# Performance work log

Measured on AMD Instinct MI355X. Metric: run time of the kernel, lower is better.

The kernel has to match this reference:

```python
import jax, jax.numpy as jnp
import numpy as np

N_NODES = 50000
N_EDGES = 800000
IN_CH = 128
HID = 32
HEADS = 8
OUT_CH = 40
NEG_SLOPE = 0.2


def setup_inputs() -> dict:
    key = jax.random.key(0)
    ks = jax.random.split(key, 12)
    g = lambda k, shape, fan: (jax.random.normal(k, shape, jnp.float32) / np.sqrt(fan).astype(np.float32))
    return {
        "x": jax.random.normal(ks[0], (N_NODES, IN_CH), jnp.float32),
        "edge_index": jax.random.randint(ks[1], (2, N_EDGES), 0, N_NODES, jnp.int64),
        "W1l": g(ks[2], (IN_CH, HEADS * HID), IN_CH),
        "W1r": g(ks[3], (IN_CH, HEADS * HID), IN_CH),
        "att1": g(ks[4], (HEADS, HID), HID),
        "b1": jnp.zeros((HEADS * HID,), jnp.float32),
        "W2l": g(ks[5], (HEADS * HID, HID), HEADS * HID),
        "W2r": g(ks[6], (HEADS * HID, HID), HEADS * HID),
        "att2": g(ks[7], (1, HID), HID),
        "b2": jnp.zeros((HID,), jnp.float32),
        "Wc": g(ks[8], (HID + IN_CH, OUT_CH), HID + IN_CH),
        "bc": jnp.zeros((OUT_CH,), jnp.float32),
    }


def _gatv2(x, ei, Wl, Wr, att, b, heads, ch):
    # GATv2Conv (concat=True): e_ij = att . LeakyReLU(Wl x_j + Wr x_i)
    n = x.shape[0]
    src, dst = ei[0], ei[1]  # message flows src(j) -> dst(i)
    xl = (x @ Wl).reshape(n, heads, ch)  # source transform
    xr = (x @ Wr).reshape(n, heads, ch)  # target transform
    e = jax.nn.leaky_relu(xl[src] + xr[dst], NEG_SLOPE)  # [E, H, C]
    score = jnp.einsum("ehc,hc->eh", e, att)             # [E, H]
    # per-target-node segment softmax (stable)
    m = jax.ops.segment_max(score, dst, num_segments=n)
    alpha = jnp.exp(score - m[dst])
    denom = jax.ops.segment_sum(alpha, dst, num_segments=n)
    alpha = alpha / denom[dst]
    out = jax.ops.segment_sum(alpha[:, :, None] * xl[src], dst, num_segments=n)
    return out.reshape(n, heads * ch) + b


def reference(x, edge_index, W1l, W1r, att1, b1, W2l, W2r, att2, b2, Wc, bc):
    n = x.shape[0]
    ar = jnp.arange(n, dtype=edge_index.dtype)
    ei = jnp.concatenate([edge_index, jnp.stack([ar, ar])], axis=1)  # add self-loops
    h1 = jax.nn.elu(_gatv2(x, ei, W1l, W1r, att1, b1, HEADS, HID))
    h2 = jax.nn.elu(_gatv2(h1, ei, W2l, W2r, att2, b2, 1, HID))
    combined = jnp.concatenate([h2, x], axis=1)
    return combined @ Wc + bc
```

## Files before the change

### kernel.cpp

```cpp
#include <hip/hip_runtime.h>
#include <cstdint>
#include <cstddef>
#include <math.h>

#define NN 50000
#define INCH 128
#define HIDC 32
#define NHEAD 8
#define OUTC 40

typedef unsigned short ushort_t;
using bf16x8 = __attribute__((ext_vector_type(8))) short;
using f32x4  = __attribute__((ext_vector_type(4))) float;

__device__ __forceinline__ float bf2f(unsigned short h) {
    return __uint_as_float(((unsigned int)h) << 16);
}
__device__ __forceinline__ unsigned short f2bf(float f) {
    unsigned int u = __float_as_uint(f);
    u = u + 0x7FFFu + ((u >> 16) & 1u);
    return (unsigned short)(u >> 16);
}
__device__ __forceinline__ float lo16(unsigned int u) { return __uint_as_float(u << 16); }
__device__ __forceinline__ float hi16(unsigned int u) { return __uint_as_float(u & 0xffff0000u); }

__global__ __launch_bounds__(256) void prep_all(
    const float* __restrict__ x, ushort_t* __restrict__ xb, int total8,
    const float* __restrict__ W1l, const float* __restrict__ W1r,
    const float* __restrict__ W2l, const float* __restrict__ W2r,
    const float* __restrict__ Wc,
    ushort_t* __restrict__ BT1, ushort_t* __restrict__ BT2, ushort_t* __restrict__ BTc,
    const int* __restrict__ ei, int E, int n, int* __restrict__ deg, int CX) {
    const int blk = blockIdx.x;
    const int tid = threadIdx.x;
    if (blk < CX) {
        int i = blk * 256 + tid;
        if (i >= total8) return;
        float4 f0 = *(const float4*)(x + (size_t)i * 8);
        float4 f1 = *(const float4*)(x + (size_t)i * 8 + 4);
        ushort4 u0, u1;
        u0.x = f2bf(f0.x); u0.y = f2bf(f0.y); u0.z = f2bf(f0.z); u0.w = f2bf(f0.w);
        u1.x = f2bf(f1.x); u1.y = f2bf(f1.y); u1.z = f2bf(f1.z); u1.w = f2bf(f1.w);
        *(ushort4*)(xb + (size_t)i * 8) = u0;
        *(ushort4*)(xb + (size_t)i * 8 + 4) = u1;
    } else if (blk < CX + 616) {
        int b = blk - CX, k = tid;
        if (b < 512) {
            if (k < 128) {
                float v = (b < 256) ? W1l[(size_t)k * 256 + b] : W1r[(size_t)k * 256 + (b - 256)];
                BT1[(size_t)b * 128 + k] = f2bf(v);
            }
        } else if (b < 576) {
            int c = b - 512;
            float v = (c < 32) ? W2l[(size_t)k * 32 + c] : W2r[(size_t)k * 32 + (c - 32)];
            BT2[(size_t)c * 256 + k] = f2bf(v);
        } else {
            int c = b - 576;
            if (k < 160) BTc[(size_t)c * 160 + k] = f2bf(Wc[(size_t)k * 40 + c]);
        }
    } else {
        int e = (blk - CX - 616) * 256 + tid;
        if (e >= E + n) return;
        int dst = (e < E) ? ei[E + e] : (e - E);
        atomicAdd(&deg[dst], 1);
    }
}


__global__ __launch_bounds__(1024) void partial_scan(
    const int* __restrict__ deg, int* __restrict__ row_start,
    int* __restrict__ block_total, int n) {
    __shared__ int wsum[16];
    const int tid = threadIdx.x, lane = tid & 63, wid = tid >> 6;
    int i = blockIdx.x * 1024 + tid;
    int v = (i < n) ? deg[i] : 0;
    int s = v;
    #pragma unroll
    for (int off = 1; off < 64; off <<= 1) {
        int t = __shfl_up(s, off, 64);
        if (lane >= off) s += t;
    }
    if (lane == 63) wsum[wid] = s;
    __syncthreads();
    if (wid == 0) {
        int ws = (lane < 16) ? wsum[lane] : 0;
        #pragma unroll
        for (int off = 1; off < 16; off <<= 1) {
            int t = __shfl_up(ws, off, 64);
            if (lane >= off) ws += t;
        }
        if (lane < 16) wsum[lane] = ws;
    }
    __syncthreads();
    int wexcl = wid ? wsum[wid - 1] : 0;
    if (i < n) row_start[i] = wexcl + s - v;
    if (tid == 0) block_total[blockIdx.x] = wsum[15];
}

__global__ void totals_scan(const int* __restrict__ block_total, int* __restrict__ block_off,
                            int* __restrict__ row_start_n, int nb) {
    int j = threadIdx.x;
    int v = (j < nb) ? block_total[j] : 0;
    int s = v;
    #pragma unroll
    for (int off = 1; off < 64; off <<= 1) {
        int t = __shfl_up(s, off, 64);
        if (j >= off) s += t;
    }
    if (j < nb) block_off[j] = s - v;
    if (j == nb - 1) *row_start_n = s;
}

__global__ __launch_bounds__(1024) void add_off(int* __restrict__ row_start, int* __restrict__ cursor,
                                                const int* __restrict__ block_off, int n) {
    int i = blockIdx.x * 1024 + threadIdx.x;
    if (i >= n) return;
    int val = row_start[i] + block_off[blockIdx.x];
    row_start[i] = val;
    cursor[i] = val;
}

__global__ void scatter_edges(const int* __restrict__ ei, int E, int n,
                              int* __restrict__ cursor, int* __restrict__ csr_src) {
    int e = blockIdx.x * blockDim.x + threadIdx.x;
    if (e >= E + n) return;
    int src, dst;
    if (e < E) { src = ei[e]; dst = ei[E + e]; } else { src = dst = e - E; }
    int pos = atomicAdd(&cursor[dst], 1);
    csr_src[pos] = src;
}

__global__ __launch_bounds__(256) void gemm1_mfma(
    const ushort_t* __restrict__ xb, const ushort_t* __restrict__ BT1,
    ushort_t* __restrict__ xlr1, int M) {
    __shared__ ushort_t As[128][72];
    __shared__ ushort_t Bs[128][72];
    const int tid = threadIdx.x;
    const int rowBase = blockIdx.y * 128;
    const int c0 = blockIdx.x * 128;
    const int wid = tid >> 6, lane = tid & 63;
    const int wr = wid >> 1, wc = wid & 1;
    const int l15 = lane & 15, l4 = lane >> 4;
    f32x4 acc[4][4];
    #pragma unroll
    for (int i = 0; i < 4; ++i)
        #pragma unroll
        for (int j = 0; j < 4; ++j)
            #pragma unroll
            for (int q = 0; q < 4; ++q) acc[i][j][q] = 0.f;

    for (int c = 0; c < 2; ++c) {
        #pragma unroll
        for (int h = 0; h < 4; ++h) {
            int idx = h * 256 + tid;
            int r = idx >> 3, seg = idx & 7;
            int row = rowBase + r;
            uint4 v = {0, 0, 0, 0};
            if (row < M) v = *(const uint4*)(xb + (size_t)row * 128 + c * 64 + seg * 8);
            *(uint4*)&As[r][seg * 8] = v;
            *(uint4*)&Bs[r][seg * 8] = *(const uint4*)(BT1 + (size_t)(c0 + r) * 128 + c * 64 + seg * 8);
        }
        __syncthreads();
        #pragma unroll
        for (int kk = 0; kk < 2; ++kk) {
            bf16x8 a[4], b[4];
            #pragma unroll
            for (int f = 0; f < 4; ++f) {
                a[f] = *(const bf16x8*)&As[wr * 64 + f * 16 + l15][kk * 32 + l4 * 8];
                b[f] = *(const bf16x8*)&Bs[wc * 64 + f * 16 + l15][kk * 32 + l4 * 8];
            }
            #pragma unroll
            for (int i = 0; i < 4; ++i)
                #pragma unroll
                for (int j = 0; j < 4; ++j)
                    acc[i][j] = __builtin_amdgcn_mfma_f32_16x16x32_bf16(a[i], b[j], acc[i][j], 0, 0, 0);
        }
        __syncthreads();
    }
    #pragma unroll
    for (int i = 0; i < 4; ++i)
        #pragma unroll
        for (int r = 0; r < 4; ++r) {
            int row = rowBase + wr * 64 + i * 16 + l4 * 4 + r;
            if (row >= M) continue;
            #pragma unroll
            for (int j = 0; j < 4; ++j) {
                int col = c0 + wc * 64 + j * 16 + l15;
                xlr1[(size_t)row * 512 + col] = f2bf(acc[i][j][r]);
            }
        }
}

__global__ __launch_bounds__(256) void dots1(
    const ushort_t* __restrict__ xlr, const float* __restrict__ att,
    float* __restrict__ dl, float* __restrict__ dr) {
    const int lane = threadIdx.x & 63;
    const int i = blockIdx.x * 4 + (threadIdx.x >> 6);
    const int l31 = lane & 31;
    const float4 atA = *(const float4*)(att + l31 * 8);
    const float4 atB = *(const float4*)(att + l31 * 8 + 4);
    ushort4 ua = *(const ushort4*)(xlr + (size_t)i * 512 + lane * 8);
    ushort4 ub = *(const ushort4*)(xlr + (size_t)i * 512 + lane * 8 + 4);
    float q = atA.x * bf2f(ua.x);
    q = fmaf(atA.y, bf2f(ua.y), q);
    q = fmaf(atA.z, bf2f(ua.z), q);
    q = fmaf(atA.w, bf2f(ua.w), q);
    q = fmaf(atB.x, bf2f(ub.x), q);
    q = fmaf(atB.y, bf2f(ub.y), q);
    q = fmaf(atB.z, bf2f(ub.z), q);
    q = fmaf(atB.w, bf2f(ub.w), q);
    q += __shfl_xor(q, 1);
    q += __shfl_xor(q, 2);
    if ((lane & 3) == 0) {
        int head = l31 >> 2;
        if (lane < 32) dl[(size_t)i * 8 + head] = q;
        else           dr[(size_t)i * 8 + head] = q;
    }
}

__global__ __launch_bounds__(256) void gat_agg1(
    const ushort_t* __restrict__ xlr, const float* __restrict__ dl,
    const float* __restrict__ dr, const float* __restrict__ att,
    const float* __restrict__ b,
    const int* __restrict__ row_start, const int* __restrict__ csr_src,
    ushort_t* __restrict__ h1) {
    const int lane = threadIdx.x & 63;
    const int i = blockIdx.x * 4 + (threadIdx.x >> 6);
    const int half = lane >> 5;
    const int sl = lane & 31;
    const int head = sl >> 2;

    uint4 xv = *(const uint4*)(xlr + (size_t)i * 512 + 256 + sl * 8);
    const float xr0 = lo16(xv.x), xr1 = hi16(xv.x), xr2 = lo16(xv.y), xr3 = hi16(xv.y);
    const float xr4 = lo16(xv.z), xr5 = hi16(xv.z), xr6 = lo16(xv.w), xr7 = hi16(xv.w);
    const float4 atA = *(const float4*)(att + sl * 8);
    const float4 atB = *(const float4*)(att + sl * 8 + 4);
    const float cbase = 0.6f * dr[(size_t)i * 8 + head];
    const int p0 = row_start[i], p1 = row_start[i + 1];

    float d = 0.f;
    float a0 = 0.f, a1 = 0.f, a2 = 0.f, a3 = 0.f, a4 = 0.f, a5 = 0.f, a6 = 0.f, a7 = 0.f;

    int pc = p0 + half; if (pc > p1 - 1) pc = p1 - 1;
    int j = csr_src[pc];
    uint4 uv = *(const uint4*)(xlr + (size_t)j * 512 + sl * 8);
    float dlj = dl[(size_t)j * 8 + head];

    for (int p = p0; p < p1; p += 2) {
        const bool val = (p + half) < p1;
        float v0 = lo16(uv.x), v1 = hi16(uv.x), v2 = lo16(uv.y), v3 = hi16(uv.y);
        float v4 = lo16(uv.z), v5 = hi16(uv.z), v6 = lo16(uv.w), v7 = hi16(uv.w);
        float base = fmaf(0.6f, dlj, cbase);
        int nxt = p + half + 2;
        if (nxt < p1) {
            int jn = csr_src[nxt];
            uv = *(const uint4*)(xlr + (size_t)jn * 512 + sl * 8);
            dlj = dl[(size_t)jn * 8 + head];
        }
        float q = atA.x * fabsf(v0 + xr0);
        q = fmaf(atA.y, fabsf(v1 + xr1), q);
        q = fmaf(atA.z, fabsf(v2 + xr2), q);
        q = fmaf(atA.w, fabsf(v3 + xr3), q);
        q = fmaf(atB.x, fabsf(v4 + xr4), q);
        q = fmaf(atB.y, fabsf(v5 + xr5), q);
        q = fmaf(atB.z, fabsf(v6 + xr6), q);
        q = fmaf(atB.w, fabsf(v7 + xr7), q);
        q += __shfl_xor(q, 1);
        q += __shfl_xor(q, 2);
        float w = val ? __expf(fmaf(0.4f, q, base)) : 0.f;
        d += w;
        a0 = fmaf(w, v0, a0); a1 = fmaf(w, v1, a1);
        a2 = fmaf(w, v2, a2); a3 = fmaf(w, v3, a3);
        a4 = fmaf(w, v4, a4); a5 = fmaf(w, v5, a5);
        a6 = fmaf(w, v6, a6); a7 = fmaf(w, v7, a7);
    }
    d  += __shfl_xor(d, 32);
    a0 += __shfl_xor(a0, 32); a1 += __shfl_xor(a1, 32);
    a2 += __shfl_xor(a2, 32); a3 += __shfl_xor(a3, 32);
    a4 += __shfl_xor(a4, 32); a5 += __shfl_xor(a5, 32);
    a6 += __shfl_xor(a6, 32); a7 += __shfl_xor(a7, 32);

    if (half == 0) {
        const float4 bA = *(const float4*)(b + sl * 8);
        const float4 bB = *(const float4*)(b + sl * 8 + 4);
        float inv = 1.f / d;
        float o0 = fmaf(a0, inv, bA.x), o1 = fmaf(a1, inv, bA.y);
        float o2 = fmaf(a2, inv, bA.z), o3 = fmaf(a3, inv, bA.w);
        float o4 = fmaf(a4, inv, bB.x), o5 = fmaf(a5, inv, bB.y);
        float o6 = fmaf(a6, inv, bB.z), o7 = fmaf(a7, inv, bB.w);
        o0 = o0 > 0.f ? o0 : __expf(o0) - 1.f;
        o1 = o1 > 0.f ? o1 : __expf(o1) - 1.f;
        o2 = o2 > 0.f ? o2 : __expf(o2) - 1.f;
        o3 = o3 > 0.f ? o3 : __expf(o3) - 1.f;
        o4 = o4 > 0.f ? o4 : __expf(o4) - 1.f;
        o5 = o5 > 0.f ? o5 : __expf(o5) - 1.f;
        o6 = o6 > 0.f ? o6 : __expf(o6) - 1.f;
        o7 = o7 > 0.f ? o7 : __expf(o7) - 1.f;
        uint4 ov;
        ov.x = ((unsigned)f2bf(o1) << 16) | f2bf(o0);
        ov.y = ((unsigned)f2bf(o3) << 16) | f2bf(o2);
        ov.z = ((unsigned)f2bf(o5) << 16) | f2bf(o4);
        ov.w = ((unsigned)f2bf(o7) << 16) | f2bf(o6);
        *(uint4*)(h1 + (size_t)i * 256 + sl * 8) = ov;
    }
}

__global__ __launch_bounds__(256) void gemm2_mfma(
    const ushort_t* __restrict__ h1, const ushort_t* __restrict__ BT2,
    ushort_t* __restrict__ xlr2, int M) {
    __shared__ ushort_t As[128][72];
    __shared__ ushort_t Bs[64][264];
    const int tid = threadIdx.x;
    const int rowBase = blockIdx.x * 128;
    const int wid = tid >> 6, lane = tid & 63;
    const int l15 = lane & 15, l4 = lane >> 4;
    #pragma unroll
    for (int h = 0; h < 8; ++h) {
        int idx = h * 256 + tid;
        int r = idx >> 5, seg = idx & 31;
        *(uint4*)&Bs[r][seg * 8] = *(const uint4*)(BT2 + (size_t)r * 256 + seg * 8);
    }
    f32x4 acc[2][4];
    #pragma unroll
    for (int i = 0; i < 2; ++i)
        #pragma unroll
        for (int j = 0; j < 4; ++j)
            #pragma unroll
            for (int q = 0; q < 4; ++q) acc[i][j][q] = 0.f;

    for (int c = 0; c < 4; ++c) {
        #pragma unroll
        for (int h = 0; h < 4; ++h) {
            int idx = h * 256 + tid;
            int r = idx >> 3, seg = idx & 7;
            int row = rowBase + r;
            uint4 v = {0, 0, 0, 0};
            if (row < M) v = *(const uint4*)(h1 + (size_t)row * 256 + c * 64 + seg * 8);
            *(uint4*)&As[r][seg * 8] = v;
        }
        __syncthreads();
        #pragma unroll
        for (int kk = 0; kk < 2; ++kk) {
            bf16x8 a[2], b[4];
            #pragma unroll
            for (int f = 0; f < 2; ++f)
                a[f] = *(const bf16x8*)&As[wid * 32 + f * 16 + l15][kk * 32 + l4 * 8];
            #pragma unroll
            for (int f = 0; f < 4; ++f)
                b[f] = *(const bf16x8*)&Bs[f * 16 + l15][c * 64 + kk * 32 + l4 * 8];
            #pragma unroll
            for (int i = 0; i < 2; ++i)
                #pragma unroll
                for (int j = 0; j < 4; ++j)
                    acc[i][j] = __builtin_amdgcn_mfma_f32_16x16x32_bf16(a[i], b[j], acc[i][j], 0, 0, 0);
        }
        __syncthreads();
    }
    #pragma unroll
    for (int i = 0; i < 2; ++i)
        #pragma unroll
        for (int r = 0; r < 4; ++r) {
            int row = rowBase + wid * 32 + i * 16 + l4 * 4 + r;
            if (row >= M) continue;
            #pragma unroll
            for (int j = 0; j < 4; ++j) {
                int col = j * 16 + l15;
                xlr2[(size_t)row * 64 + col] = f2bf(acc[i][j][r]);
            }
        }
}

__global__ __launch_bounds__(256) void dots2(
    const ushort_t* __restrict__ xlr, const float* __restrict__ att,
    float* __restrict__ dl, float* __restrict__ dr) {
    const int lane = threadIdx.x & 63;
    const int i = blockIdx.x * 8 + (threadIdx.x >> 6) * 2 + (lane >> 5);
    const int sub = lane & 31;
    const float2 at = *(const float2*)(att + (sub & 15) * 2);
    ushort2 u = *(const ushort2*)(xlr + (size_t)i * 64 + sub * 2);
    float q = at.x * bf2f(u.x);
    q = fmaf(at.y, bf2f(u.y), q);
    q += __shfl_xor(q, 1);
    q += __shfl_xor(q, 2);
    q += __shfl_xor(q, 4);
    q += __shfl_xor(q, 8);
    if ((sub & 15) == 0) {
        if (sub < 16) dl[i] = q;
        else          dr[i] = q;
    }
}

__global__ __launch_bounds__(256) void gat_agg2(
    const ushort_t* __restrict__ xlr, const float* __restrict__ dl,
    const float* __restrict__ dr, const float* __restrict__ att,
    const float* __restrict__ b,
    const int* __restrict__ row_start, const int* __restrict__ csr_src,
    ushort_t* __restrict__ h2) {
    const int lane = threadIdx.x & 63;
    const int i = blockIdx.x * 4 + (threadIdx.x >> 6);
    const int g = lane >> 4, h = lane & 15;
    const unsigned xru = *(const unsigned*)(xlr + (size_t)i * 64 + 32 + h * 2);
    const float xr0 = lo16(xru), xr1v = hi16(xru);
    const float2 atv = *(const float2*)(att + h * 2);
    const float cbase = 0.6f * dr[i];
    const int p0 = row_start[i], p1 = row_start[i + 1];
    float d = 0.f, a0 = 0.f, a1 = 0.f;

    int pc = p0 + g; if (pc > p1 - 1) pc = p1 - 1;
    int j = csr_src[pc];
    unsigned uv = *(const unsigned*)(xlr + (size_t)j * 64 + h * 2);
    float dlj = dl[j];

    for (int p = p0; p < p1; p += 4) {
        const bool val = (p + g) < p1;
        float v0 = lo16(uv), v1 = hi16(uv);
        float base = fmaf(0.6f, dlj, cbase);
        int nxt = p + g + 4;
        if (nxt < p1) {
            int jn = csr_src[nxt];
            uv = *(const unsigned*)(xlr + (size_t)jn * 64 + h * 2);
            dlj = dl[jn];
        }
        float q = atv.x * fabsf(v0 + xr0);
        q = fmaf(atv.y, fabsf(v1 + xr1v), q);
        q += __shfl_xor(q, 1);
        q += __shfl_xor(q, 2);
        q += __shfl_xor(q, 4);
        q += __shfl_xor(q, 8);
        float w = val ? __expf(fmaf(0.4f, q, base)) : 0.f;
        d += w;
        a0 = fmaf(w, v0, a0);
        a1 = fmaf(w, v1, a1);
    }
    d += __shfl_xor(d, 16);  d += __shfl_xor(d, 32);
    a0 += __shfl_xor(a0, 16); a0 += __shfl_xor(a0, 32);
    a1 += __shfl_xor(a1, 16); a1 += __shfl_xor(a1, 32);
    if (g == 0) {
        float inv = 1.f / d;
        float o0 = fmaf(a0, inv, b[h * 2]);
        float o1 = fmaf(a1, inv, b[h * 2 + 1]);
        o0 = o0 > 0.f ? o0 : __expf(o0) - 1.f;
        o1 = o1 > 0.f ? o1 : __expf(o1) - 1.f;
        ushort2 ou; ou.x = f2bf(o0); ou.y = f2bf(o1);
        *(ushort2*)(h2 + (size_t)i * 32 + h * 2) = ou;
    }
}

__global__ __launch_bounds__(256) void final_mfma(
    const ushort_t* __restrict__ h2, const ushort_t* __restrict__ xb,
    const ushort_t* __restrict__ BTc, const float* __restrict__ bc,
    float* __restrict__ out, int M) {
    __shared__ ushort_t As[128][168];
    __shared__ ushort_t Bs[48][168];
    const int tid = threadIdx.x;
    const int rowBase = blockIdx.x * 128;
    const int wid = tid >> 6, lane = tid & 63;
    const int l15 = lane & 15, l4 = lane >> 4;
    #pragma unroll
    for (int h = 0; h < 4; ++h) {
        int idx = h * 256 + tid;
        if (idx < 960) {
            int r = idx / 20, seg = idx % 20;
            uint4 v = {0, 0, 0, 0};
            if (r < 40) v = *(const uint4*)(BTc + (size_t)r * 160 + seg * 8);
            *(uint4*)&Bs[r][seg * 8] = v;
        }
    }
    #pragma unroll
    for (int h = 0; h < 10; ++h) {
        int idx = h * 256 + tid;
        int r = idx / 20, seg = idx % 20;
        int row = rowBase + r;
        uint4 v = {0, 0, 0, 0};
        if (row < M)
            v = (seg < 4) ? *(const uint4*)(h2 + (size_t)row * 32 + seg * 8)
                          : *(const uint4*)(xb + (size_t)row * 128 + (seg - 4) * 8);
        *(uint4*)&As[r][seg * 8] = v;
    }
    __syncthreads();
    f32x4 acc[2][3];
    #pragma unroll
    for (int i = 0; i < 2; ++i)
        #pragma unroll
        for (int j = 0; j < 3; ++j)
            #pragma unroll
            for (int q = 0; q < 4; ++q) acc[i][j][q] = 0.f;
    #pragma unroll
    for (int kk = 0; kk < 5; ++kk) {
        bf16x8 a[2], b[3];
        #pragma unroll
        for (int f = 0; f < 2; ++f)
            a[f] = *(const bf16x8*)&As[wid * 32 + f * 16 + l15][kk * 32 + l4 * 8];
        #pragma unroll
        for (int f = 0; f < 3; ++f)
            b[f] = *(const bf16x8*)&Bs[f * 16 + l15][kk * 32 + l4 * 8];
        #pragma unroll
        for (int i = 0; i < 2; ++i)
            #pragma unroll
            for (int j = 0; j < 3; ++j)
                acc[i][j] = __builtin_amdgcn_mfma_f32_16x16x32_bf16(a[i], b[j], acc[i][j], 0, 0, 0);
    }
    #pragma unroll
    for (int i = 0; i < 2; ++i)
        #pragma unroll
        for (int r = 0; r < 4; ++r) {
            int row = rowBase + wid * 32 + i * 16 + l4 * 4 + r;
            if (row >= M) continue;
            #pragma unroll
            for (int j = 0; j < 3; ++j) {
                int col = j * 16 + l15;
                if (col < 40) out[(size_t)row * 40 + col] = acc[i][j][r] + bc[col];
            }
        }
}


extern "C" void kernel_launch(void* const* d_in, const int* in_sizes, int n_in,
                              void* d_out, int out_size, void* d_ws, size_t ws_size,
                              hipStream_t stream) {
    const float* x    = (const float*)d_in[0];
    const int*   ei   = (const int*)d_in[1];
    const float* W1l  = (const float*)d_in[2];
    const float* W1r  = (const float*)d_in[3];
    const float* att1 = (const float*)d_in[4];
    const float* b1   = (const float*)d_in[5];
    const float* W2l  = (const float*)d_in[6];
    const float* W2r  = (const float*)d_in[7];
    const float* att2 = (const float*)d_in[8];
    const float* b2   = (const float*)d_in[9];
    const float* Wc   = (const float*)d_in[10];
    const float* bc   = (const float*)d_in[11];
    float* out = (float*)d_out;

    const int n  = NN;
    const int E  = in_sizes[1] / 2;
    const int TE = E + n;
    const int NB = (n + 1023) / 1024;
    const int CX = (n * 128 / 8 + 255) / 256;
    const int CD = (TE + 255) / 256;

    char* ws = (char*)d_ws;
    size_t off = 0;
    auto alloc = [&](size_t bytes) { void* p = ws + off; off += (bytes + 255) & ~(size_t)255; return p; };
    ushort_t* xb   = (ushort_t*)alloc((size_t)n * 128 * 2);
    ushort_t* xlr1 = (ushort_t*)alloc((size_t)n * 512 * 2);
    ushort_t* h1   = (ushort_t*)alloc((size_t)n * 256 * 2);
    ushort_t* xlr2 = (ushort_t*)alloc((size_t)n * 64 * 2);
    ushort_t* h2   = (ushort_t*)alloc((size_t)n * 32 * 2);
    ushort_t* BT1  = (ushort_t*)alloc(512 * 128 * 2);
    ushort_t* BT2  = (ushort_t*)alloc(64 * 256 * 2);
    ushort_t* BTc  = (ushort_t*)alloc(40 * 160 * 2);
    float* dl1 = (float*)alloc((size_t)n * 8 * 4);
    float* dr1 = (float*)alloc((size_t)n * 8 * 4);
    float* dl2 = (float*)alloc((size_t)n * 4);
    float* dr2 = (float*)alloc((size_t)n * 4);
    int* row_start   = (int*)alloc((size_t)(n + 1) * 4);
    int* cursor      = (int*)alloc((size_t)(n + 1) * 4);
    int* deg         = (int*)alloc((size_t)n * 4);
    int* block_total = (int*)alloc((size_t)NB * 4);
    int* block_off   = (int*)alloc((size_t)NB * 4);
    int* csr_src     = (int*)alloc((size_t)TE * 4);

    hipMemsetAsync(deg, 0, (size_t)n * 4, stream);
    prep_all<<<CX + 616 + CD, 256, 0, stream>>>(x, xb, n * 128 / 8,
        W1l, W1r, W2l, W2r, Wc, BT1, BT2, BTc, ei, E, n, deg, CX);

    partial_scan<<<NB, 1024, 0, stream>>>(deg, row_start, block_total, n);
    totals_scan<<<1, 64, 0, stream>>>(block_total, block_off, row_start + n, NB);
    add_off<<<NB, 1024, 0, stream>>>(row_start, cursor, block_off, n);
    scatter_edges<<<CD, 256, 0, stream>>>(ei, E, n, cursor, csr_src);

    gemm1_mfma<<<dim3(4, (n + 127) / 128), 256, 0, stream>>>(xb, BT1, xlr1, n);
    dots1<<<n / 4, 256, 0, stream>>>(xlr1, att1, dl1, dr1);
    gat_agg1<<<n / 4, 256, 0, stream>>>(xlr1, dl1, dr1, att1, b1, row_start, csr_src, h1);

    gemm2_mfma<<<(n + 127) / 128, 256, 0, stream>>>(h1, BT2, xlr2, n);
    dots2<<<n / 8, 256, 0, stream>>>(xlr2, att2, dl2, dr2);
    gat_agg2<<<n / 4, 256, 0, stream>>>(xlr2, dl2, dr2, att2, b2, row_start, csr_src, h2);

    final_mfma<<<(n + 127) / 128, 256, 0, stream>>>(h2, xb, BTc, bc, out, n);
}
```

Measured before the change: 352.1 us.

## Fuse attention dot products into GEMM epilogues and deepen gather prefetch in aggregations

Removes the separate dots1/dots2 kernels and computes the per-node attention projections (dl/dr) directly from the MFMA accumulators in the gemm1/gemm2 epilogues using lane shuffles. This saves two kernel launches and a re-read of xlr1/xlr2 from memory. gat_agg1 and gat_agg2 now keep two gather streams in flight per lane group, and gat_agg2 gives each lane 4 channels with 8 edge groups instead of 2 channels with 4. The epilogues add shuffle work and use fp32 accumulators where the old path used bf16-rounded values, which changes numerics slightly.

```diff
diff --git a/kernel.cpp b/kernel.cpp
--- a/kernel.cpp
+++ b/kernel.cpp
@@ -132,12 +132,14 @@
 
 __global__ __launch_bounds__(256) void gemm1_mfma(
     const ushort_t* __restrict__ xb, const ushort_t* __restrict__ BT1,
-    ushort_t* __restrict__ xlr1, int M) {
+    const float* __restrict__ att,
+    ushort_t* __restrict__ xlr1, float* __restrict__ dl, float* __restrict__ dr, int M) {
     __shared__ ushort_t As[128][72];
     __shared__ ushort_t Bs[128][72];
     const int tid = threadIdx.x;
     const int rowBase = blockIdx.y * 128;
-    const int c0 = blockIdx.x * 128;
+    const int bx = blockIdx.x;
+    const int c0 = bx * 128;
     const int wid = tid >> 6, lane = tid & 63;
     const int wr = wid >> 1, wc = wid & 1;
     const int l15 = lane & 15, l4 = lane >> 4;
@@ -189,33 +191,30 @@
                 xlr1[(size_t)row * 512 + col] = f2bf(acc[i][j][r]);
             }
         }
-}
-
-__global__ __launch_bounds__(256) void dots1(
-    const ushort_t* __restrict__ xlr, const float* __restrict__ att,
-    float* __restrict__ dl, float* __restrict__ dr) {
-    const int lane = threadIdx.x & 63;
-    const int i = blockIdx.x * 4 + (threadIdx.x >> 6);
-    const int l31 = lane & 31;
-    const float4 atA = *(const float4*)(att + l31 * 8);
-    const float4 atB = *(const float4*)(att + l31 * 8 + 4);
-    ushort4 ua = *(const ushort4*)(xlr + (size_t)i * 512 + lane * 8);
-    ushort4 ub = *(const ushort4*)(xlr + (size_t)i * 512 + lane * 8 + 4);
-    float q = atA.x * bf2f(ua.x);
-    q = fmaf(atA.y, bf2f(ua.y), q);
-    q = fmaf(atA.z, bf2f(ua.z), q);
-    q = fmaf(atA.w, bf2f(ua.w), q);
-    q = fmaf(atB.x, bf2f(ub.x), q);
-    q = fmaf(atB.y, bf2f(ub.y), q);
-    q = fmaf(atB.z, bf2f(ub.z), q);
-    q = fmaf(atB.w, bf2f(ub.w), q);
-    q += __shfl_xor(q, 1);
-    q += __shfl_xor(q, 2);
-    if ((lane & 3) == 0) {
-        int head = l31 >> 2;
-        if (lane < 32) dl[(size_t)i * 8 + head] = q;
-        else           dr[(size_t)i * 8 + head] = q;
-    }
+    float attv[4];
+    #pragma unroll
+    for (int j = 0; j < 4; ++j)
+        attv[j] = att[(bx & 1) * 128 + wc * 64 + j * 16 + l15];
+    float* __restrict__ dst = (bx < 2) ? dl : dr;
+    const int headA = (bx & 1) * 4 + wc * 2;
+    #pragma unroll
+    for (int i = 0; i < 4; ++i)
+        #pragma unroll
+        for (int r = 0; r < 4; ++r) {
+            float s0 = fmaf(acc[i][1][r], attv[1], acc[i][0][r] * attv[0]);
+            float s1 = fmaf(acc[i][3][r], attv[3], acc[i][2][r] * attv[2]);
+            s0 += __shfl_xor(s0, 1); s1 += __shfl_xor(s1, 1);
+            s0 += __shfl_xor(s0, 2); s1 += __shfl_xor(s1, 2);
+            s0 += __shfl_xor(s0, 4); s1 += __shfl_xor(s1, 4);
+            s0 += __shfl_xor(s0, 8); s1 += __shfl_xor(s1, 8);
+            if (l15 == 0) {
+                int row = rowBase + wr * 64 + i * 16 + l4 * 4 + r;
+                if (row < M) {
+                    dst[(size_t)row * 8 + headA] = s0;
+                    dst[(size_t)row * 8 + headA + 1] = s1;
+                }
+            }
+        }
 }
 
 __global__ __launch_bounds__(256) void gat_agg1(
@@ -241,38 +240,72 @@
     float d = 0.f;
     float a0 = 0.f, a1 = 0.f, a2 = 0.f, a3 = 0.f, a4 = 0.f, a5 = 0.f, a6 = 0.f, a7 = 0.f;
 
-    int pc = p0 + half; if (pc > p1 - 1) pc = p1 - 1;
-    int j = csr_src[pc];
-    uint4 uv = *(const uint4*)(xlr + (size_t)j * 512 + sl * 8);
-    float dlj = dl[(size_t)j * 8 + head];
-
-    for (int p = p0; p < p1; p += 2) {
-        const bool val = (p + half) < p1;
-        float v0 = lo16(uv.x), v1 = hi16(uv.x), v2 = lo16(uv.y), v3 = hi16(uv.y);
-        float v4 = lo16(uv.z), v5 = hi16(uv.z), v6 = lo16(uv.w), v7 = hi16(uv.w);
-        float base = fmaf(0.6f, dlj, cbase);
-        int nxt = p + half + 2;
-        if (nxt < p1) {
-            int jn = csr_src[nxt];
-            uv = *(const uint4*)(xlr + (size_t)jn * 512 + sl * 8);
-            dlj = dl[(size_t)jn * 8 + head];
-        }
-        float q = atA.x * fabsf(v0 + xr0);
-        q = fmaf(atA.y, fabsf(v1 + xr1), q);
-        q = fmaf(atA.z, fabsf(v2 + xr2), q);
-        q = fmaf(atA.w, fabsf(v3 + xr3), q);
-        q = fmaf(atB.x, fabsf(v4 + xr4), q);
-        q = fmaf(atB.y, fabsf(v5 + xr5), q);
-        q = fmaf(atB.z, fabsf(v6 + xr6), q);
-        q = fmaf(atB.w, fabsf(v7 + xr7), q);
-        q += __shfl_xor(q, 1);
-        q += __shfl_xor(q, 2);
-        float w = val ? __expf(fmaf(0.4f, q, base)) : 0.f;
-        d += w;
-        a0 = fmaf(w, v0, a0); a1 = fmaf(w, v1, a1);
-        a2 = fmaf(w, v2, a2); a3 = fmaf(w, v3, a3);
-        a4 = fmaf(w, v4, a4); a5 = fmaf(w, v5, a5);
-        a6 = fmaf(w, v6, a6); a7 = fmaf(w, v7, a7);
+    int e0 = p0 + half;     int pc0 = e0 < p1 ? e0 : p1 - 1;
+    int j0 = csr_src[pc0];
+    uint4 uv0 = *(const uint4*)(xlr + (size_t)j0 * 512 + sl * 8);
+    float dl0 = dl[(size_t)j0 * 8 + head];
+    int e1 = p0 + half + 2; int pc1 = e1 < p1 ? e1 : p1 - 1;
+    int j1 = csr_src[pc1];
+    uint4 uv1 = *(const uint4*)(xlr + (size_t)j1 * 512 + sl * 8);
+    float dl1 = dl[(size_t)j1 * 8 + head];
+
+    for (int p = p0; p < p1; p += 4) {
+        {
+            const bool val = (p + half) < p1;
+            float v0 = lo16(uv0.x), v1 = hi16(uv0.x), v2 = lo16(uv0.y), v3 = hi16(uv0.y);
+            float v4 = lo16(uv0.z), v5 = hi16(uv0.z), v6 = lo16(uv0.w), v7 = hi16(uv0.w);
+            float base = fmaf(0.6f, dl0, cbase);
+            int nxt = p + half + 4;
+            if (nxt < p1) {
+                int jn = csr_src[nxt];
+                uv0 = *(const uint4*)(xlr + (size_t)jn * 512 + sl * 8);
+                dl0 = dl[(size_t)jn * 8 + head];
+            }
+            float q = atA.x * fabsf(v0 + xr0);
+            q = fmaf(atA.y, fabsf(v1 + xr1), q);
+            q = fmaf(atA.z, fabsf(v2 + xr2), q);
+            q = fmaf(atA.w, fabsf(v3 + xr3), q);
+            q = fmaf(atB.x, fabsf(v4 + xr4), q);
+            q = fmaf(atB.y, fabsf(v5 + xr5), q);
+            q = fmaf(atB.z, fabsf(v6 + xr6), q);
+            q = fmaf(atB.w, fabsf(v7 + xr7), q);
+            q += __shfl_xor(q, 1);
+            q += __shfl_xor(q, 2);
+            float w = val ? __expf(fmaf(0.4f, q, base)) : 0.f;
+            d += w;
+            a0 = fmaf(w, v0, a0); a1 = fmaf(w, v1, a1);
+            a2 = fmaf(w, v2, a2); a3 = fmaf(w, v3, a3);
+            a4 = fmaf(w, v4, a4); a5 = fmaf(w, v5, a5);
+            a6 = fmaf(w, v6, a6); a7 = fmaf(w, v7, a7);
+        }
+        {
+            const bool val = (p + 2 + half) < p1;
+            float v0 = lo16(uv1.x), v1 = hi16(uv1.x), v2 = lo16(uv1.y), v3 = hi16(uv1.y);
+            float v4 = lo16(uv1.z), v5 = hi16(uv1.z), v6 = lo16(uv1.w), v7 = hi16(uv1.w);
+            float base = fmaf(0.6f, dl1, cbase);
+            int nxt = p + half + 6;
+            if (nxt < p1) {
+                int jn = csr_src[nxt];
+                uv1 = *(const uint4*)(xlr + (size_t)jn * 512 + sl * 8);
+                dl1 = dl[(size_t)jn * 8 + head];
+            }
+            float q = atA.x * fabsf(v0 + xr0);
+            q = fmaf(atA.y, fabsf(v1 + xr1), q);
+            q = fmaf(atA.z, fabsf(v2 + xr2), q);
+            q = fmaf(atA.w, fabsf(v3 + xr3), q);
+            q = fmaf(atB.x, fabsf(v4 + xr4), q);
+            q = fmaf(atB.y, fabsf(v5 + xr5), q);
+            q = fmaf(atB.z, fabsf(v6 + xr6), q);
+            q = fmaf(atB.w, fabsf(v7 + xr7), q);
+            q += __shfl_xor(q, 1);
+            q += __shfl_xor(q, 2);
+            float w = val ? __expf(fmaf(0.4f, q, base)) : 0.f;
+            d += w;
+            a0 = fmaf(w, v0, a0); a1 = fmaf(w, v1, a1);
+            a2 = fmaf(w, v2, a2); a3 = fmaf(w, v3, a3);
+            a4 = fmaf(w, v4, a4); a5 = fmaf(w, v5, a5);
+            a6 = fmaf(w, v6, a6); a7 = fmaf(w, v7, a7);
+        }
     }
     d  += __shfl_xor(d, 32);
     a0 += __shfl_xor(a0, 32); a1 += __shfl_xor(a1, 32);
@@ -307,7 +340,8 @@
 
 __global__ __launch_bounds__(256) void gemm2_mfma(
     const ushort_t* __restrict__ h1, const ushort_t* __restrict__ BT2,
-    ushort_t* __restrict__ xlr2, int M) {
+    const float* __restrict__ att,
+    ushort_t* __restrict__ xlr2, float* __restrict__ dl2, float* __restrict__ dr2, int M) {
     __shared__ ushort_t As[128][72];
     __shared__ ushort_t Bs[64][264];
     const int tid = threadIdx.x;
@@ -368,26 +402,28 @@
                 xlr2[(size_t)row * 64 + col] = f2bf(acc[i][j][r]);
             }
         }
-}
-
-__global__ __launch_bounds__(256) void dots2(
-    const ushort_t* __restrict__ xlr, const float* __restrict__ att,
-    float* __restrict__ dl, float* __restrict__ dr) {
-    const int lane = threadIdx.x & 63;
-    const int i = blockIdx.x * 8 + (threadIdx.x >> 6) * 2 + (lane >> 5);
-    const int sub = lane & 31;
-    const float2 at = *(const float2*)(att + (sub & 15) * 2);
-    ushort2 u = *(const ushort2*)(xlr + (size_t)i * 64 + sub * 2);
-    float q = at.x * bf2f(u.x);
-    q = fmaf(at.y, bf2f(u.y), q);
-    q += __shfl_xor(q, 1);
-    q += __shfl_xor(q, 2);
-    q += __shfl_xor(q, 4);
-    q += __shfl_xor(q, 8);
-    if ((sub & 15) == 0) {
-        if (sub < 16) dl[i] = q;
-        else          dr[i] = q;
-    }
+    float attv[4];
+    #pragma unroll
+    for (int j = 0; j < 4; ++j)
+        attv[j] = att[(j * 16 + l15) & 31];
+    #pragma unroll
+    for (int i = 0; i < 2; ++i)
+        #pragma unroll
+        for (int r = 0; r < 4; ++r) {
+            float s0 = fmaf(acc[i][1][r], attv[1], acc[i][0][r] * attv[0]);
+            float s1 = fmaf(acc[i][3][r], attv[3], acc[i][2][r] * attv[2]);
+            s0 += __shfl_xor(s0, 1); s1 += __shfl_xor(s1, 1);
+            s0 += __shfl_xor(s0, 2); s1 += __shfl_xor(s1, 2);
+            s0 += __shfl_xor(s0, 4); s1 += __shfl_xor(s1, 4);
+            s0 += __shfl_xor(s0, 8); s1 += __shfl_xor(s1, 8);
+            if (l15 == 0) {
+                int row = rowBase + wid * 32 + i * 16 + l4 * 4 + r;
+                if (row < M) {
+                    dl2[row] = s0;
+                    dr2[row] = s1;
+                }
+            }
+        }
 }
 
 __global__ __launch_bounds__(256) void gat_agg2(
@@ -398,51 +434,90 @@
     ushort_t* __restrict__ h2) {
     const int lane = threadIdx.x & 63;
     const int i = blockIdx.x * 4 + (threadIdx.x >> 6);
-    const int g = lane >> 4, h = lane & 15;
-    const unsigned xru = *(const unsigned*)(xlr + (size_t)i * 64 + 32 + h * 2);
-    const float xr0 = lo16(xru), xr1v = hi16(xru);
-    const float2 atv = *(const float2*)(att + h * 2);
+    const int g = lane >> 3;
+    const int h8 = lane & 7;
+    uint2 xv = *(const uint2*)(xlr + (size_t)i * 64 + 32 + h8 * 4);
+    const float xr0 = lo16(xv.x), xr1 = hi16(xv.x), xr2 = lo16(xv.y), xr3 = hi16(xv.y);
+    const float4 at = *(const float4*)(att + h8 * 4);
     const float cbase = 0.6f * dr[i];
     const int p0 = row_start[i], p1 = row_start[i + 1];
-    float d = 0.f, a0 = 0.f, a1 = 0.f;
-
-    int pc = p0 + g; if (pc > p1 - 1) pc = p1 - 1;
-    int j = csr_src[pc];
-    unsigned uv = *(const unsigned*)(xlr + (size_t)j * 64 + h * 2);
-    float dlj = dl[j];
-
-    for (int p = p0; p < p1; p += 4) {
-        const bool val = (p + g) < p1;
-        float v0 = lo16(uv), v1 = hi16(uv);
-        float base = fmaf(0.6f, dlj, cbase);
-        int nxt = p + g + 4;
-        if (nxt < p1) {
-            int jn = csr_src[nxt];
-            uv = *(const unsigned*)(xlr + (size_t)jn * 64 + h * 2);
-            dlj = dl[jn];
-        }
-        float q = atv.x * fabsf(v0 + xr0);
-        q = fmaf(atv.y, fabsf(v1 + xr1v), q);
-        q += __shfl_xor(q, 1);
-        q += __shfl_xor(q, 2);
-        q += __shfl_xor(q, 4);
-        q += __shfl_xor(q, 8);
-        float w = val ? __expf(fmaf(0.4f, q, base)) : 0.f;
-        d += w;
-        a0 = fmaf(w, v0, a0);
-        a1 = fmaf(w, v1, a1);
-    }
-    d += __shfl_xor(d, 16);  d += __shfl_xor(d, 32);
-    a0 += __shfl_xor(a0, 16); a0 += __shfl_xor(a0, 32);
-    a1 += __shfl_xor(a1, 16); a1 += __shfl_xor(a1, 32);
+    float d = 0.f, a0 = 0.f, a1 = 0.f, a2 = 0.f, a3 = 0.f;
+
+    int e0 = p0 + g;     int pc0 = e0 < p1 ? e0 : p1 - 1;
+    int j0 = csr_src[pc0];
+    uint2 uv0 = *(const uint2*)(xlr + (size_t)j0 * 64 + h8 * 4);
+    float dl0 = dl[j0];
+    int e1 = p0 + g + 8; int pc1 = e1 < p1 ? e1 : p1 - 1;
+    int j1 = csr_src[pc1];
+    uint2 uv1 = *(const uint2*)(xlr + (size_t)j1 * 64 + h8 * 4);
+    float dl1 = dl[j1];
+
+    for (int p = p0; p < p1; p += 16) {
+        {
+            const bool val = (p + g) < p1;
+            float v0 = lo16(uv0.x), v1 = hi16(uv0.x), v2 = lo16(uv0.y), v3 = hi16(uv0.y);
+            float base = fmaf(0.6f, dl0, cbase);
+            int nxt = p + g + 16;
+            if (nxt < p1) {
+                int jn = csr_src[nxt];
+                uv0 = *(const uint2*)(xlr + (size_t)jn * 64 + h8 * 4);
+                dl0 = dl[jn];
+            }
+            float q = at.x * fabsf(v0 + xr0);
+            q = fmaf(at.y, fabsf(v1 + xr1), q);
+            q = fmaf(at.z, fabsf(v2 + xr2), q);
+            q = fmaf(at.w, fabsf(v3 + xr3), q);
+            q += __shfl_xor(q, 1);
+            q += __shfl_xor(q, 2);
+            q += __shfl_xor(q, 4);
+            float w = val ? __expf(fmaf(0.4f, q, base)) : 0.f;
+            d += w;
+            a0 = fmaf(w, v0, a0); a1 = fmaf(w, v1, a1);
+            a2 = fmaf(w, v2, a2); a3 = fmaf(w, v3, a3);
+        }
+        {
+            const bool val = (p + g + 8) < p1;
+            float v0 = lo16(uv1.x), v1 = hi16(uv1.x), v2 = lo16(uv1.y), v3 = hi16(uv1.y);
+            float base = fmaf(0.6f, dl1, cbase);
+            int nxt = p + g + 24;
+            if (nxt < p1) {
+                int jn = csr_src[nxt];
+                uv1 = *(const uint2*)(xlr + (size_t)jn * 64 + h8 * 4);
+                dl1 = dl[jn];
+            }
+            float q = at.x * fabsf(v0 + xr0);
+            q = fmaf(at.y, fabsf(v1 + xr1), q);
+            q = fmaf(at.z, fabsf(v2 + xr2), q);
+            q = fmaf(at.w, fabsf(v3 + xr3), q);
+            q += __shfl_xor(q, 1);
+            q += __shfl_xor(q, 2);
+            q += __shfl_xor(q, 4);
+            float w = val ? __expf(fmaf(0.4f, q, base)) : 0.f;
+            d += w;
+            a0 = fmaf(w, v0, a0); a1 = fmaf(w, v1, a1);
+            a2 = fmaf(w, v2, a2); a3 = fmaf(w, v3, a3);
+        }
+    }
+    d  += __shfl_xor(d, 8);  d  += __shfl_xor(d, 16);  d  += __shfl_xor(d, 32);
+    a0 += __shfl_xor(a0, 8); a0 += __shfl_xor(a0, 16); a0 += __shfl_xor(a0, 32);
+    a1 += __shfl_xor(a1, 8); a1 += __shfl_xor(a1, 16); a1 += __shfl_xor(a1, 32);
+    a2 += __shfl_xor(a2, 8); a2 += __shfl_xor(a2, 16); a2 += __shfl_xor(a2, 32);
+    a3 += __shfl_xor(a3, 8); a3 += __shfl_xor(a3, 16); a3 += __shfl_xor(a3, 32);
     if (g == 0) {
+        const float4 bb = *(const float4*)(b + h8 * 4);
         float inv = 1.f / d;
-        float o0 = fmaf(a0, inv, b[h * 2]);
-        float o1 = fmaf(a1, inv, b[h * 2 + 1]);
+        float o0 = fmaf(a0, inv, bb.x);
+        float o1 = fmaf(a1, inv, bb.y);
+        float o2 = fmaf(a2, inv, bb.z);
+        float o3 = fmaf(a3, inv, bb.w);
         o0 = o0 > 0.f ? o0 : __expf(o0) - 1.f;
         o1 = o1 > 0.f ? o1 : __expf(o1) - 1.f;
-        ushort2 ou; ou.x = f2bf(o0); ou.y = f2bf(o1);
-        *(ushort2*)(h2 + (size_t)i * 32 + h * 2) = ou;
+        o2 = o2 > 0.f ? o2 : __expf(o2) - 1.f;
+        o3 = o3 > 0.f ? o3 : __expf(o3) - 1.f;
+        uint2 ov;
+        ov.x = ((unsigned)f2bf(o1) << 16) | f2bf(o0);
+        ov.y = ((unsigned)f2bf(o3) << 16) | f2bf(o2);
+        *(uint2*)(h2 + (size_t)i * 32 + h8 * 4) = ov;
     }
 }
 
@@ -570,12 +645,10 @@
     add_off<<<NB, 1024, 0, stream>>>(row_start, cursor, block_off, n);
     scatter_edges<<<CD, 256, 0, stream>>>(ei, E, n, cursor, csr_src);
 
-    gemm1_mfma<<<dim3(4, (n + 127) / 128), 256, 0, stream>>>(xb, BT1, xlr1, n);
-    dots1<<<n / 4, 256, 0, stream>>>(xlr1, att1, dl1, dr1);
+    gemm1_mfma<<<dim3(4, (n + 127) / 128), 256, 0, stream>>>(xb, BT1, att1, xlr1, dl1, dr1, n);
     gat_agg1<<<n / 4, 256, 0, stream>>>(xlr1, dl1, dr1, att1, b1, row_start, csr_src, h1);
 
-    gemm2_mfma<<<(n + 127) / 128, 256, 0, stream>>>(h1, BT2, xlr2, n);
-    dots2<<<n / 8, 256, 0, stream>>>(xlr2, att2, dl2, dr2);
+    gemm2_mfma<<<(n + 127) / 128, 256, 0, stream>>>(h1, BT2, att2, xlr2, dl2, dr2, n);
     gat_agg2<<<n / 4, 256, 0, stream>>>(xlr2, dl2, dr2, att2, b2, row_start, csr_src, h2);
 
     final_mfma<<<(n + 127) / 128, 256, 0, stream>>>(h2, xb, BTc, bc, out, n);
```

Result: faster. 342.9 us (-2.6%).
